# Performance work log

Measured on AMD Instinct MI355X. Metric: run time of the kernel, lower is better.

Reference implementation:

```python
import jax, jax.numpy as jnp
import numpy as np

N_NODES = 20000
N_ATTRS = 5000
IN_FEATURES = 512
OUT_FEATURES = 128
ALPHA = 0.2  # LeakyReLU negative slope
NEG_INF = -9e15


def setup_inputs() -> dict:
    key = jax.random.key(0)
    k1, k2, k3, k4, k5 = jax.random.split(key, 5)
    node_embedding = jax.random.normal(k1, (N_NODES, IN_FEATURES), dtype=jnp.float32)
    attr_embedding = jax.random.normal(k2, (N_ATTRS, IN_FEATURES), dtype=jnp.float32)
    feat_mat = jax.random.randint(k3, (N_NODES, N_ATTRS), 0, 2, dtype=jnp.int32)
    # xavier_uniform with gain=1.414 (as in torch init)
    gain = 1.414
    lim_W = gain * np.sqrt(6.0 / (IN_FEATURES + OUT_FEATURES))
    W = jax.random.uniform(k4, (IN_FEATURES, OUT_FEATURES), minval=-lim_W, maxval=lim_W, dtype=jnp.float32)
    lim_a = gain * np.sqrt(6.0 / (2 * OUT_FEATURES + 1))
    a = jax.random.uniform(k5, (2 * OUT_FEATURES, 1), minval=-lim_a, maxval=lim_a, dtype=jnp.float32)
    return {"node_embedding": node_embedding, "attr_embedding": attr_embedding,
            "feat_mat": feat_mat, "W": W, "a": a}


def reference(node_embedding, attr_embedding, feat_mat, W, a):
    # Linear projections
    node_h = node_embedding @ W            # [N, F]
    attr_h = attr_embedding @ W            # [M, F]
    # Additive attention scores: e[i,j] = leakyrelu(a1.node_h[i] + a2.attr_h[j])
    wh1 = node_h @ a[:OUT_FEATURES, :]     # [N, 1]
    wh2 = attr_h @ a[OUT_FEATURES:, :]     # [M, 1]
    e = jax.nn.leaky_relu(wh1 + wh2.T, negative_slope=ALPHA)  # [N, M]
    # Mask where there is no node-attribute link, then softmax over attrs
    attention = jnp.where(feat_mat > 0, e, NEG_INF)
    attention = jax.nn.softmax(attention, axis=1)
    # (dropout is identity in eval mode)
    h_prime = attention @ attr_h           # [N, F]
    return jax.nn.elu(h_prime)             # concat=True branch
```

## Files before the change

kernel.cpp:

```cpp
#include <hip/hip_runtime.h>

#define N_NODES 20000
#define N_ATTRS 5000
#define IN_F    512
#define OUT_F   128
#define KP      5120
#define KSTEPS  (KP / 32)
#define LOG2E   1.4426950408889634f

typedef _Float16 f16x8 __attribute__((ext_vector_type(8)));
typedef float    f32x4 __attribute__((ext_vector_type(4)));

__device__ __forceinline__ float fast_exp2(float x) {
    return __builtin_amdgcn_exp2f(x);
}

__global__ __launch_bounds__(256) void prep_kernel(
    const float* __restrict__ W, const float* __restrict__ a,
    float* __restrict__ Wa1, float* __restrict__ Wa2, _Float16* __restrict__ Wp) {
    int gt = blockIdx.x * blockDim.x + threadIdx.x;
    if (gt < IN_F) {
        int k = gt;
        float s1 = 0.f, s2 = 0.f;
        for (int f = 0; f < OUT_F; ++f) {
            float w = W[k * OUT_F + f];
            s1 += w * a[f];
            s2 += w * a[OUT_F + f];
        }
        Wa1[k] = s1 * LOG2E;
        Wa2[k] = s2 * LOG2E;
    }
    for (int idx = gt; idx < IN_F * OUT_F; idx += gridDim.x * blockDim.x) {
        int j    = idx & 7;
        int lane = (idx >> 3) & 63;
        int nb   = (idx >> 9) & 7;
        int kb   = idx >> 12;
        int k = kb * 32 + (lane >> 4) * 8 + j;
        int n = nb * 16 + (lane & 15);
        Wp[idx] = (_Float16)W[k * OUT_F + n];
    }
}

__global__ __launch_bounds__(256) void wh_kernel(
    const float* __restrict__ node_emb, const float* __restrict__ attr_emb,
    const float* __restrict__ Wa1, const float* __restrict__ Wa2,
    float* __restrict__ wh1, float* __restrict__ wh2) {
    int wave = threadIdx.x >> 6, lane = threadIdx.x & 63;
    int r = blockIdx.x * 4 + wave;
    const float* src;
    const float* vec;
    float* dst;
    if (r < N_NODES) {
        src = node_emb + (size_t)r * IN_F; vec = Wa1; dst = wh1 + r;
    } else {
        int r2 = r - N_NODES;
        src = attr_emb + (size_t)r2 * IN_F; vec = Wa2; dst = wh2 + r2;
    }
    float4 ra = *reinterpret_cast<const float4*>(src + lane * 8);
    float4 rb = *reinterpret_cast<const float4*>(src + lane * 8 + 4);
    const float* vp = vec + lane * 8;
    float s = ra.x * vp[0] + ra.y * vp[1] + ra.z * vp[2] + ra.w * vp[3]
            + rb.x * vp[4] + rb.y * vp[5] + rb.z * vp[6] + rb.w * vp[7];
#pragma unroll
    for (int off = 1; off < 64; off <<= 1) s += __shfl_xor(s, off, 64);
    if (lane == 0) *dst = s;
}

__global__ __launch_bounds__(256) void max_kernel(
    float* __restrict__ wh2, float* __restrict__ maxp) {
    __shared__ float red[4];
    int t = threadIdx.x;
    float m = -1e30f;
    for (int j = t; j < N_ATTRS; j += 256) m = fmaxf(m, wh2[j]);
    if (t < KP - N_ATTRS) wh2[N_ATTRS + t] = 0.f;
#pragma unroll
    for (int off = 1; off < 64; off <<= 1) m = fmaxf(m, __shfl_xor(m, off, 64));
    int wave = t >> 6, lane = t & 63;
    if (lane == 0) red[wave] = m;
    __syncthreads();
    if (t == 0) *maxp = fmaxf(fmaxf(red[0], red[1]), fmaxf(red[2], red[3]));
}

__global__ __launch_bounds__(256) void attr_h_kernel(
    const float* __restrict__ attr_emb, const _Float16* __restrict__ Wp,
    _Float16* __restrict__ Vp) {
    int wave = threadIdx.x >> 6, lane = threadIdx.x & 63;
    int m = lane & 15, quad = lane >> 4;
    int j0 = (blockIdx.x * 4 + wave) * 16;
    int j = j0 + m;
    bool valid = j < N_ATTRS;
    f32x4 acc[8];
#pragma unroll
    for (int nb = 0; nb < 8; ++nb)
#pragma unroll
        for (int t = 0; t < 4; ++t) acc[nb][t] = 0.f;
    const float* arow = attr_emb + (size_t)j * IN_F;
    for (int kk = 0; kk < IN_F / 32; ++kk) {
        f16x8 afrag;
        if (valid) {
            float4 ra = *reinterpret_cast<const float4*>(arow + kk * 32 + quad * 8);
            float4 rb = *reinterpret_cast<const float4*>(arow + kk * 32 + quad * 8 + 4);
            afrag[0] = (_Float16)ra.x; afrag[1] = (_Float16)ra.y;
            afrag[2] = (_Float16)ra.z; afrag[3] = (_Float16)ra.w;
            afrag[4] = (_Float16)rb.x; afrag[5] = (_Float16)rb.y;
            afrag[6] = (_Float16)rb.z; afrag[7] = (_Float16)rb.w;
        } else {
#pragma unroll
            for (int t = 0; t < 8; ++t) afrag[t] = (_Float16)0.f;
        }
        const _Float16* wbase = Wp + (size_t)(kk * 8) * 64 * 8;
#pragma unroll
        for (int nb = 0; nb < 8; ++nb) {
            f16x8 bfrag;
            __builtin_memcpy(&bfrag, wbase + (nb * 64 + lane) * 8, 16);
            acc[nb] = __builtin_amdgcn_mfma_f32_16x16x32_f16(afrag, bfrag, acc[nb], 0, 0, 0);
        }
    }
#pragma unroll
    for (int nb = 0; nb < 8; ++nb) {
#pragma unroll
        for (int reg = 0; reg < 4; ++reg) {
            int jr = j0 + quad * 4 + reg;
            int n = nb * 16 + m;
            float v = (jr < N_ATTRS) ? acc[nb][reg] : 0.f;
            size_t idx = ((size_t)((jr >> 5) * 8 + nb) * 64 +
                          (((jr >> 3) & 3) * 16 + m)) * 8 + (jr & 7);
            Vp[idx] = (_Float16)v;
        }
    }
}

__global__ __launch_bounds__(256, 2) void attn_kernel(
    const int* __restrict__ feat, const float* __restrict__ wh1,
    const float* __restrict__ wh2, const float* __restrict__ maxwh2,
    const _Float16* __restrict__ Vp, float* __restrict__ out) {
    __shared__ float accs[4][16][128];
    __shared__ float rsums[4][16];

    int wave = threadIdx.x >> 6, lane = threadIdx.x & 63;
    int m = lane & 15, quad = lane >> 4;
    int i0 = blockIdx.x * 16;
    int i = i0 + m;
    float wh1i = wh1[i];
    float emax = wh1i + maxwh2[0];
    float Mi = fmaxf(emax, 0.2f * emax) - 12.f;
    const int* frow = feat + (size_t)i * N_ATTRS;

    f32x4 acc[8];
#pragma unroll
    for (int nb = 0; nb < 8; ++nb)
#pragma unroll
        for (int t = 0; t < 4; ++t) acc[nb][t] = 0.f;
    float s = 0.f;

    int kk0 = wave * (KSTEPS / 4);
    int kk1 = kk0 + (KSTEPS / 4);
    for (int kk = kk0; kk < kk1; ++kk) {
        int jb = kk * 32 + quad * 8;
        int4 f0 = {0, 0, 0, 0}, f1 = {0, 0, 0, 0};
        if (jb < N_ATTRS) {
            f0 = *reinterpret_cast<const int4*>(frow + jb);
            f1 = *reinterpret_cast<const int4*>(frow + jb + 4);
        }
        float4 w2a = *reinterpret_cast<const float4*>(wh2 + jb);
        float4 w2b = *reinterpret_cast<const float4*>(wh2 + jb + 4);
        int   fi[8] = {f0.x, f0.y, f0.z, f0.w, f1.x, f1.y, f1.z, f1.w};
        float w2[8] = {w2a.x, w2a.y, w2a.z, w2a.w, w2b.x, w2b.y, w2b.z, w2b.w};
        f16x8 afrag;
#pragma unroll
        for (int t = 0; t < 8; ++t) {
            float e = wh1i + w2[t];
            float l = fmaxf(e, 0.2f * e);
            float p = fast_exp2(l - Mi);
            p = (fi[t] > 0) ? p : 0.f;
            _Float16 ph = (_Float16)p;
            s += (float)ph;
            afrag[t] = ph;
        }
        const _Float16* vbase = Vp + (size_t)(kk * 8) * 64 * 8;
#pragma unroll
        for (int nb = 0; nb < 8; ++nb) {
            f16x8 bfrag;
            __builtin_memcpy(&bfrag, vbase + (nb * 64 + lane) * 8, 16);
            acc[nb] = __builtin_amdgcn_mfma_f32_16x16x32_f16(afrag, bfrag, acc[nb], 0, 0, 0);
        }
    }

    s += __shfl_xor(s, 16, 64);
    s += __shfl_xor(s, 32, 64);
    if (lane < 16) rsums[wave][lane] = s;

#pragma unroll
    for (int nb = 0; nb < 8; ++nb)
#pragma unroll
        for (int reg = 0; reg < 4; ++reg)
            accs[wave][quad * 4 + reg][nb * 16 + m] = acc[nb][reg];

    __syncthreads();

    for (int o = threadIdx.x; o < 16 * 128; o += 256) {
        int lr = o >> 7, n = o & 127;
        float v = accs[0][lr][n] + accs[1][lr][n] + accs[2][lr][n] + accs[3][lr][n];
        float rs = rsums[0][lr] + rsums[1][lr] + rsums[2][lr] + rsums[3][lr];
        rs = (rs > 0.f) ? rs : 1.f;
        float h = v / rs;
        float ov = (h > 0.f) ? h : (fast_exp2(h * LOG2E) - 1.f);
        out[(size_t)(i0 + lr) * OUT_F + n] = ov;
    }
}

extern "C" void kernel_launch(void* const* d_in, const int* in_sizes, int n_in,
                              void* d_out, int out_size, void* d_ws, size_t ws_size,
                              hipStream_t stream) {
    const float* node_emb = (const float*)d_in[0];
    const float* attr_emb = (const float*)d_in[1];
    const int*   feat     = (const int*)d_in[2];
    const float* W        = (const float*)d_in[3];
    const float* a        = (const float*)d_in[4];
    float*       out      = (float*)d_out;

    char* ws = (char*)d_ws;
    float*    Wa1 = (float*)(ws + 0);
    float*    Wa2 = (float*)(ws + 4096);
    float*    wh1 = (float*)(ws + 8192);
    float*    wh2 = (float*)(ws + 90112);
    float*    mx  = (float*)(ws + 110592);
    _Float16* Wp  = (_Float16*)(ws + 131072);
    _Float16* Vp  = (_Float16*)(ws + 262144);

    prep_kernel<<<64, 256, 0, stream>>>(W, a, Wa1, Wa2, Wp);
    wh_kernel<<<6250, 256, 0, stream>>>(node_emb, attr_emb, Wa1, Wa2, wh1, wh2);
    max_kernel<<<1, 256, 0, stream>>>(wh2, mx);
    attr_h_kernel<<<80, 256, 0, stream>>>(attr_emb, Wp, Vp);
    attn_kernel<<<1250, 256, 0, stream>>>(feat, wh1, wh2, mx, Vp, out);
}
```

Baseline: 693.8 us.

## Shrink attention LDS, raise occupancy, and prefetch next feat/wh2 tile

The cross-wave reduction in the attention kernel now accumulates into a single padded 16x132 LDS tile, with waves adding in turn between barriers, instead of four separate per-wave buffers. This cuts shared memory per block so launch bounds can request four blocks per CU instead of two. The main loop also software-prefetches the next iteration's feat_mat and wh2 loads into registers. The wh2 padding is widened so the prefetch reads stay in bounds, and the max scalar is moved to make room. The serialized reduction adds three extra barriers, and the prefetch adds register pressure under a tighter register budget.

```diff
diff --git a/kernel.cpp b/kernel.cpp
--- a/kernel.cpp
+++ b/kernel.cpp
@@ -6,6 +6,7 @@
 #define OUT_F   128
 #define KP      5120
 #define KSTEPS  (KP / 32)
+#define WH2_PAD 5376
 #define LOG2E   1.4426950408889634f
 
 typedef _Float16 f16x8 __attribute__((ext_vector_type(8)));
@@ -72,7 +73,7 @@
     int t = threadIdx.x;
     float m = -1e30f;
     for (int j = t; j < N_ATTRS; j += 256) m = fmaxf(m, wh2[j]);
-    if (t < KP - N_ATTRS) wh2[N_ATTRS + t] = 0.f;
+    for (int j = N_ATTRS + t; j < WH2_PAD; j += 256) wh2[j] = 0.f;
 #pragma unroll
     for (int off = 1; off < 64; off <<= 1) m = fmaxf(m, __shfl_xor(m, off, 64));
     int wave = t >> 6, lane = t & 63;
@@ -130,12 +131,12 @@
     }
 }
 
-__global__ __launch_bounds__(256, 2) void attn_kernel(
+__global__ __launch_bounds__(256, 4) void attn_kernel(
     const int* __restrict__ feat, const float* __restrict__ wh1,
     const float* __restrict__ wh2, const float* __restrict__ maxwh2,
     const _Float16* __restrict__ Vp, float* __restrict__ out) {
-    __shared__ float accs[4][16][128];
-    __shared__ float rsums[4][16];
+    __shared__ float accs[16][132];
+    __shared__ float rsums[16];
 
     int wave = threadIdx.x >> 6, lane = threadIdx.x & 63;
     int m = lane & 15, quad = lane >> 4;
@@ -155,15 +156,31 @@
 
     int kk0 = wave * (KSTEPS / 4);
     int kk1 = kk0 + (KSTEPS / 4);
+
+    int jb = kk0 * 32 + quad * 8;
+    int4 f0 = {0, 0, 0, 0}, f1 = {0, 0, 0, 0};
+    if (jb < N_ATTRS) {
+        f0 = *reinterpret_cast<const int4*>(frow + jb);
+        f1 = *reinterpret_cast<const int4*>(frow + jb + 4);
+    }
+    float4 w2a = *reinterpret_cast<const float4*>(wh2 + jb);
+    float4 w2b = *reinterpret_cast<const float4*>(wh2 + jb + 4);
+
+    const _Float16* vbase = Vp + (size_t)(kk0 * 8) * 64 * 8;
+
     for (int kk = kk0; kk < kk1; ++kk) {
-        int jb = kk * 32 + quad * 8;
-        int4 f0 = {0, 0, 0, 0}, f1 = {0, 0, 0, 0};
-        if (jb < N_ATTRS) {
-            f0 = *reinterpret_cast<const int4*>(frow + jb);
-            f1 = *reinterpret_cast<const int4*>(frow + jb + 4);
-        }
-        float4 w2a = *reinterpret_cast<const float4*>(wh2 + jb);
-        float4 w2b = *reinterpret_cast<const float4*>(wh2 + jb + 4);
+        int jbn = jb + 32;
+        int4 nf0 = {0, 0, 0, 0}, nf1 = {0, 0, 0, 0};
+        float4 nw2a = {0.f, 0.f, 0.f, 0.f}, nw2b = {0.f, 0.f, 0.f, 0.f};
+        if (kk + 1 < kk1) {
+            if (jbn < N_ATTRS) {
+                nf0 = *reinterpret_cast<const int4*>(frow + jbn);
+                nf1 = *reinterpret_cast<const int4*>(frow + jbn + 4);
+            }
+            nw2a = *reinterpret_cast<const float4*>(wh2 + jbn);
+            nw2b = *reinterpret_cast<const float4*>(wh2 + jbn + 4);
+        }
+
         int   fi[8] = {f0.x, f0.y, f0.z, f0.w, f1.x, f1.y, f1.z, f1.w};
         float w2[8] = {w2a.x, w2a.y, w2a.z, w2a.w, w2b.x, w2b.y, w2b.z, w2b.w};
         f16x8 afrag;
@@ -177,31 +194,47 @@
             s += (float)ph;
             afrag[t] = ph;
         }
-        const _Float16* vbase = Vp + (size_t)(kk * 8) * 64 * 8;
+
 #pragma unroll
         for (int nb = 0; nb < 8; ++nb) {
             f16x8 bfrag;
             __builtin_memcpy(&bfrag, vbase + (nb * 64 + lane) * 8, 16);
             acc[nb] = __builtin_amdgcn_mfma_f32_16x16x32_f16(afrag, bfrag, acc[nb], 0, 0, 0);
         }
+
+        f0 = nf0; f1 = nf1; w2a = nw2a; w2b = nw2b; jb = jbn;
+        vbase += 8 * 64 * 8;
     }
 
     s += __shfl_xor(s, 16, 64);
     s += __shfl_xor(s, 32, 64);
-    if (lane < 16) rsums[wave][lane] = s;
-
-#pragma unroll
-    for (int nb = 0; nb < 8; ++nb)
-#pragma unroll
-        for (int reg = 0; reg < 4; ++reg)
-            accs[wave][quad * 4 + reg][nb * 16 + m] = acc[nb][reg];
-
-    __syncthreads();
+
+#pragma unroll
+    for (int w = 0; w < 4; ++w) {
+        if (wave == w) {
+            if (w == 0) {
+#pragma unroll
+                for (int nb = 0; nb < 8; ++nb)
+#pragma unroll
+                    for (int reg = 0; reg < 4; ++reg)
+                        accs[quad * 4 + reg][nb * 16 + m] = acc[nb][reg];
+                if (lane < 16) rsums[lane] = s;
+            } else {
+#pragma unroll
+                for (int nb = 0; nb < 8; ++nb)
+#pragma unroll
+                    for (int reg = 0; reg < 4; ++reg)
+                        accs[quad * 4 + reg][nb * 16 + m] += acc[nb][reg];
+                if (lane < 16) rsums[lane] += s;
+            }
+        }
+        __syncthreads();
+    }
 
     for (int o = threadIdx.x; o < 16 * 128; o += 256) {
         int lr = o >> 7, n = o & 127;
-        float v = accs[0][lr][n] + accs[1][lr][n] + accs[2][lr][n] + accs[3][lr][n];
-        float rs = rsums[0][lr] + rsums[1][lr] + rsums[2][lr] + rsums[3][lr];
+        float v = accs[lr][n];
+        float rs = rsums[lr];
         rs = (rs > 0.f) ? rs : 1.f;
         float h = v / rs;
         float ov = (h > 0.f) ? h : (fast_exp2(h * LOG2E) - 1.f);
@@ -224,7 +257,7 @@
     float*    Wa2 = (float*)(ws + 4096);
     float*    wh1 = (float*)(ws + 8192);
     float*    wh2 = (float*)(ws + 90112);
-    float*    mx  = (float*)(ws + 110592);
+    float*    mx  = (float*)(ws + 111616);
     _Float16* Wp  = (_Float16*)(ws + 131072);
     _Float16* Vp  = (_Float16*)(ws + 262144);
 
```

After: 689.5 us. Within noise of the previous version (-0.6%).

## Double-buffer V, feat and wh2 tiles in LDS via async global-to-LDS loads

Applied to the files above, without the earlier changes.

The attention kernel now handles 32 node rows per block, with wave pairs splitting the attribute range. V, feat and wh2 tiles are staged into LDS with global_load_lds and double buffered so the next stage loads while the current one computes. Each V tile in LDS is reused by two row groups, and the padding is changed to -1e30 so out-of-range attributes give zero weight. This adds a block barrier every step and raises LDS use to about 50KB, which may limit occupancy. Grid size and launch bounds change to match.

```diff
diff --git a/kernel.cpp b/kernel.cpp
--- a/kernel.cpp
+++ b/kernel.cpp
@@ -5,14 +5,24 @@
 #define IN_F    512
 #define OUT_F   128
 #define KP      5120
-#define KSTEPS  (KP / 32)
+#define KSTEPS  160
+#define NSS     80
+#define WH2_PAD 5376
+#define NEGBIG  -1e30f
 #define LOG2E   1.4426950408889634f
 
 typedef _Float16 f16x8 __attribute__((ext_vector_type(8)));
 typedef float    f32x4 __attribute__((ext_vector_type(4)));
+typedef int      i32x4 __attribute__((ext_vector_type(4)));
 
 __device__ __forceinline__ float fast_exp2(float x) {
     return __builtin_amdgcn_exp2f(x);
+}
+
+__device__ __forceinline__ void async16(void* lds_dst, const void* gsrc) {
+    __builtin_amdgcn_global_load_lds(
+        (const __attribute__((address_space(1))) unsigned int*)gsrc,
+        (__attribute__((address_space(3))) unsigned int*)lds_dst, 16, 0, 0);
 }
 
 __global__ __launch_bounds__(256) void prep_kernel(
@@ -72,7 +82,7 @@
     int t = threadIdx.x;
     float m = -1e30f;
     for (int j = t; j < N_ATTRS; j += 256) m = fmaxf(m, wh2[j]);
-    if (t < KP - N_ATTRS) wh2[N_ATTRS + t] = 0.f;
+    for (int j = N_ATTRS + t; j < WH2_PAD; j += 256) wh2[j] = NEGBIG;
 #pragma unroll
     for (int off = 1; off < 64; off <<= 1) m = fmaxf(m, __shfl_xor(m, off, 64));
     int wave = t >> 6, lane = t & 63;
@@ -130,21 +140,22 @@
     }
 }
 
-__global__ __launch_bounds__(256, 2) void attn_kernel(
+__global__ __launch_bounds__(256, 3) void attn_kernel(
     const int* __restrict__ feat, const float* __restrict__ wh1,
     const float* __restrict__ wh2, const float* __restrict__ maxwh2,
     const _Float16* __restrict__ Vp, float* __restrict__ out) {
-    __shared__ float accs[4][16][128];
-    __shared__ float rsums[4][16];
+    __shared__ __align__(16) char lds[49664];
+    __shared__ float rsums[32];
 
     int wave = threadIdx.x >> 6, lane = threadIdx.x & 63;
     int m = lane & 15, quad = lane >> 4;
-    int i0 = blockIdx.x * 16;
-    int i = i0 + m;
-    float wh1i = wh1[i];
+    int i0 = blockIdx.x * 32;
+    int rg = (wave >> 1) * 16;
+    int half = wave & 1;
+
+    float wh1i = wh1[i0 + rg + m];
     float emax = wh1i + maxwh2[0];
     float Mi = fmaxf(emax, 0.2f * emax) - 12.f;
-    const int* frow = feat + (size_t)i * N_ATTRS;
 
     f32x4 acc[8];
 #pragma unroll
@@ -153,23 +164,50 @@
         for (int t = 0; t < 4; ++t) acc[nb][t] = 0.f;
     float s = 0.f;
 
-    int kk0 = wave * (KSTEPS / 4);
-    int kk1 = kk0 + (KSTEPS / 4);
-    for (int kk = kk0; kk < kk1; ++kk) {
-        int jb = kk * 32 + quad * 8;
-        int4 f0 = {0, 0, 0, 0}, f1 = {0, 0, 0, 0};
-        if (jb < N_ATTRS) {
-            f0 = *reinterpret_cast<const int4*>(frow + jb);
-            f1 = *reinterpret_cast<const int4*>(frow + jb + 4);
-        }
-        float4 w2a = *reinterpret_cast<const float4*>(wh2 + jb);
-        float4 w2b = *reinterpret_cast<const float4*>(wh2 + jb + 4);
-        int   fi[8] = {f0.x, f0.y, f0.z, f0.w, f1.x, f1.y, f1.z, f1.w};
-        float w2[8] = {w2a.x, w2a.y, w2a.z, w2a.w, w2b.x, w2b.y, w2b.z, w2b.w};
+    char* vbuf0 = lds;
+    char* fbuf0 = lds + 32768;
+    char* wbuf0 = lds + 49152;
+
+    const char* featb = (const char*)feat;
+    size_t frow_off = (size_t)(i0 + rg + m) * N_ATTRS * 4;
+
+    auto stage = [&](int ss, int b) {
+        const char* vsrc = (const char*)Vp + (size_t)ss * 16384 + wave * 4096 + lane * 16;
+        char* vdst = vbuf0 + b * 16384 + wave * 4096;
+#pragma unroll
+        for (int q = 0; q < 4; ++q) async16(vdst + q * 1024, vsrc + q * 1024);
+        int kbase = (2 * ss + half) * 32;
+        char* fdst = fbuf0 + b * 8192 + wave * 2048;
+#pragma unroll
+        for (int h = 0; h < 2; ++h) {
+            int a = kbase + quad * 8 + h * 4;
+            a = min(a, N_ATTRS - 4);
+            async16(fdst + h * 1024, featb + frow_off + (size_t)a * 4);
+        }
+        if (wave == 0 && lane < 16)
+            async16(wbuf0 + b * 256, (const char*)(wh2 + ss * 64) + lane * 16);
+    };
+
+    stage(0, 0);
+    __syncthreads();
+
+    for (int ss = 0; ss < NSS; ++ss) {
+        int cur = ss & 1;
+        if (ss + 1 < NSS) stage(ss + 1, cur ^ 1);
+
+        char* wb = wbuf0 + cur * 256 + half * 128 + quad * 32;
+        float4 wva = *reinterpret_cast<const float4*>(wb);
+        float4 wvb = *reinterpret_cast<const float4*>(wb + 16);
+        char* fb = fbuf0 + cur * 8192 + wave * 2048 + lane * 16;
+        i32x4 fA = *reinterpret_cast<const i32x4*>(fb);
+        i32x4 fB = *reinterpret_cast<const i32x4*>(fb + 1024);
+
+        int   fi[8] = {fA.x, fA.y, fA.z, fA.w, fB.x, fB.y, fB.z, fB.w};
+        float wv[8] = {wva.x, wva.y, wva.z, wva.w, wvb.x, wvb.y, wvb.z, wvb.w};
         f16x8 afrag;
 #pragma unroll
         for (int t = 0; t < 8; ++t) {
-            float e = wh1i + w2[t];
+            float e = wh1i + wv[t];
             float l = fmaxf(e, 0.2f * e);
             float p = fast_exp2(l - Mi);
             p = (fi[t] > 0) ? p : 0.f;
@@ -177,31 +215,44 @@
             s += (float)ph;
             afrag[t] = ph;
         }
-        const _Float16* vbase = Vp + (size_t)(kk * 8) * 64 * 8;
+
+        char* vb = vbuf0 + cur * 16384 + half * 8192;
 #pragma unroll
         for (int nb = 0; nb < 8; ++nb) {
-            f16x8 bfrag;
-            __builtin_memcpy(&bfrag, vbase + (nb * 64 + lane) * 8, 16);
+            f16x8 bfrag = *reinterpret_cast<const f16x8*>(vb + nb * 1024 + lane * 16);
             acc[nb] = __builtin_amdgcn_mfma_f32_16x16x32_f16(afrag, bfrag, acc[nb], 0, 0, 0);
         }
+
+        __syncthreads();
     }
 
     s += __shfl_xor(s, 16, 64);
     s += __shfl_xor(s, 32, 64);
-    if (lane < 16) rsums[wave][lane] = s;
-
-#pragma unroll
-    for (int nb = 0; nb < 8; ++nb)
-#pragma unroll
-        for (int reg = 0; reg < 4; ++reg)
-            accs[wave][quad * 4 + reg][nb * 16 + m] = acc[nb][reg];
-
-    __syncthreads();
-
-    for (int o = threadIdx.x; o < 16 * 128; o += 256) {
+
+    float* accp = (float*)lds;
+    if (half == 0) {
+#pragma unroll
+        for (int nb = 0; nb < 8; ++nb)
+#pragma unroll
+            for (int reg = 0; reg < 4; ++reg)
+                accp[(rg + quad * 4 + reg) * 128 + nb * 16 + m] = acc[nb][reg];
+        if (lane < 16) rsums[rg + lane] = s;
+    }
+    __syncthreads();
+    if (half == 1) {
+#pragma unroll
+        for (int nb = 0; nb < 8; ++nb)
+#pragma unroll
+            for (int reg = 0; reg < 4; ++reg)
+                accp[(rg + quad * 4 + reg) * 128 + nb * 16 + m] += acc[nb][reg];
+        if (lane < 16) rsums[rg + lane] += s;
+    }
+    __syncthreads();
+
+    for (int o = threadIdx.x; o < 32 * 128; o += 256) {
         int lr = o >> 7, n = o & 127;
-        float v = accs[0][lr][n] + accs[1][lr][n] + accs[2][lr][n] + accs[3][lr][n];
-        float rs = rsums[0][lr] + rsums[1][lr] + rsums[2][lr] + rsums[3][lr];
+        float v = accp[lr * 128 + n];
+        float rs = rsums[lr];
         rs = (rs > 0.f) ? rs : 1.f;
         float h = v / rs;
         float ov = (h > 0.f) ? h : (fast_exp2(h * LOG2E) - 1.f);
@@ -224,7 +275,7 @@
     float*    Wa2 = (float*)(ws + 4096);
     float*    wh1 = (float*)(ws + 8192);
     float*    wh2 = (float*)(ws + 90112);
-    float*    mx  = (float*)(ws + 110592);
+    float*    mx  = (float*)(ws + 111616);
     _Float16* Wp  = (_Float16*)(ws + 131072);
     _Float16* Vp  = (_Float16*)(ws + 262144);
 
@@ -232,5 +283,5 @@
     wh_kernel<<<6250, 256, 0, stream>>>(node_emb, attr_emb, Wa1, Wa2, wh1, wh2);
     max_kernel<<<1, 256, 0, stream>>>(wh2, mx);
     attr_h_kernel<<<80, 256, 0, stream>>>(attr_emb, Wp, Vp);
-    attn_kernel<<<1250, 256, 0, stream>>>(feat, wh1, wh2, mx, Vp, out);
-}
+    attn_kernel<<<625, 256, 0, stream>>>(feat, wh1, wh2, mx, Vp, out);
+}
```

Measured after the change: 649.9 us. -6.3%, faster.
